# Kernel optimization log

Hardware: AMD Instinct MI355X
Metric: run time of the kernel (lower is better)

Reference implementation:

```python
import jax, jax.numpy as jnp
import numpy as np

D_MODEL = 1024
H = 16
D_K = D_MODEL // H
THETA = 10000.0
MAX_SEQ = 2048
SEQ = 2048
BATCH = 2


def _rope_tables():
    # tri[i, k] angles: i / theta**(2k/d_k)
    pos = jnp.arange(MAX_SEQ, dtype=jnp.float32)[:, None]          # [S, 1]
    inv_freq = THETA ** (-2.0 * jnp.arange(D_K // 2, dtype=jnp.float32) / D_K)  # [dk/2]
    ang = pos * inv_freq                                            # [S, dk/2]
    return jnp.cos(ang), jnp.sin(ang)


def _apply_rope(x, token_positions, cos_t, sin_t):
    # x: [b, h, s, dk]; rotate interleaved pairs
    cos = cos_t[token_positions]  # [s, dk/2]
    sin = sin_t[token_positions]
    x2 = x.reshape(x.shape[:-1] + (D_K // 2, 2))
    x0, x1 = x2[..., 0], x2[..., 1]
    r0 = x0 * cos - x1 * sin
    r1 = x0 * sin + x1 * cos
    return jnp.stack([r0, r1], axis=-1).reshape(x.shape)


def setup_inputs() -> dict:
    key = jax.random.key(0)
    ks = jax.random.split(key, 5)
    sigma = np.sqrt(2.0 / (D_MODEL + D_MODEL))
    return {
        "x": jax.random.normal(ks[0], (BATCH, SEQ, D_MODEL), dtype=jnp.float32),
        "token_positions": jnp.arange(SEQ, dtype=jnp.int64 if jax.config.jax_enable_x64 else jnp.int32),
        "Wq": (jax.random.normal(ks[1], (D_MODEL, D_MODEL), dtype=jnp.float32) * sigma),
        "Wk": (jax.random.normal(ks[2], (D_MODEL, D_MODEL), dtype=jnp.float32) * sigma),
        "Wv": (jax.random.normal(ks[3], (D_MODEL, D_MODEL), dtype=jnp.float32) * sigma),
        "Wo": (jax.random.normal(ks[4], (D_MODEL, D_MODEL), dtype=jnp.float32) * sigma),
    }


def reference(x, token_positions, Wq, Wk, Wv, Wo):
    b, s, _ = x.shape
    cos_t, sin_t = _rope_tables()

    def proj(W):
        y = jnp.einsum('oi,bsi->bso', W, x)                 # [b, s, d_model]
        return y.reshape(b, s, H, D_K).transpose(0, 2, 1, 3)  # [b, h, s, dk]

    Q = _apply_rope(proj(Wq), token_positions, cos_t, sin_t)
    K = _apply_rope(proj(Wk), token_positions, cos_t, sin_t)
    V = proj(Wv)

    scores = jnp.einsum('bhqd,bhkd->bhqk', Q, K) / jnp.sqrt(jnp.float32(D_K))
    causal = jnp.tril(jnp.ones((s, s), dtype=bool))
    scores = jnp.where(causal, scores, -jnp.inf)
    attn = jax.nn.softmax(scores, axis=-1)
    out = jnp.einsum('bhqk,bhkd->bhqd', attn, V)            # [b, h, s, dv]
    out = out.transpose(0, 2, 1, 3).reshape(b, s, D_MODEL)
    return jnp.einsum('oi,bsi->bso', Wo, out)
```

## Files before the change

kernel.cpp:

```cpp
#include <hip/hip_runtime.h>
#include <hip/hip_bf16.h>
#include <math.h>

#define D_MODEL 1024
#define NH      16
#define DK      64
#define SEQ     2048
#define BATCH   2

typedef float  f32x4  __attribute__((ext_vector_type(4)));
typedef __bf16 bf16x8 __attribute__((ext_vector_type(8)));
typedef unsigned short ushx4 __attribute__((ext_vector_type(4)));
typedef unsigned short ushx8 __attribute__((ext_vector_type(8)));
typedef unsigned short u16;

__device__ inline u16 cbf(float f) { __bf16 h = (__bf16)f; return *(u16*)&h; }

__device__ inline void gload16(const u16* g, u16* l) {
    __builtin_amdgcn_global_load_lds(
        (const __attribute__((address_space(1))) unsigned int*)g,
        (__attribute__((address_space(3))) unsigned int*)l,
        16, 0, 0);
}

__global__ void rope_tables_kernel(float* __restrict__ cost, float* __restrict__ sint) {
    int i = blockIdx.x * 256 + threadIdx.x;
    int pos = i >> 5, k = i & 31;
    float inv = powf(10000.0f, -2.0f * (float)k / 64.0f);
    float ang = (float)pos * inv;
    cost[i] = cosf(ang);
    sint[i] = sinf(ang);
}

__global__ void cvt_kernel(const float* __restrict__ in, u16* __restrict__ out) {
    size_t i = ((size_t)blockIdx.x * 256 + threadIdx.x) * 8;
    f32x4 v0 = *(const f32x4*)(in + i);
    f32x4 v1 = *(const f32x4*)(in + i + 4);
    ushx4 o0, o1;
    #pragma unroll
    for (int e = 0; e < 4; e++) { o0[e] = cbf(v0[e]); o1[e] = cbf(v1[e]); }
    *(ushx4*)(out + i) = o0;
    *(ushx4*)(out + i + 4) = o1;
}

__global__ void cvtw_kernel(const float* __restrict__ wq, const float* __restrict__ wk,
                            const float* __restrict__ wv, const float* __restrict__ wo,
                            u16* __restrict__ oq, u16* __restrict__ ok,
                            u16* __restrict__ ov, u16* __restrict__ oo) {
    const float* in; u16* out;
    switch (blockIdx.y) {
        case 0: in = wq; out = oq; break;
        case 1: in = wk; out = ok; break;
        case 2: in = wv; out = ov; break;
        default: in = wo; out = oo; break;
    }
    size_t i = ((size_t)blockIdx.x * 256 + threadIdx.x) * 8;
    f32x4 v0 = *(const f32x4*)(in + i);
    f32x4 v1 = *(const f32x4*)(in + i + 4);
    ushx4 o0, o1;
    #pragma unroll
    for (int e = 0; e < 4; e++) { o0[e] = cbf(v0[e]); o1[e] = cbf(v1[e]); }
    *(ushx4*)(out + i) = o0;
    *(ushx4*)(out + i + 4) = o1;
}

__global__ __launch_bounds__(256) void gemm_qkv(
    const u16* __restrict__ A, const u16* __restrict__ Wqkv,
    u16* __restrict__ Qo, u16* __restrict__ Ko, u16* __restrict__ Vo,
    const int* __restrict__ tpos,
    const float* __restrict__ cost, const float* __restrict__ sint)
{
    constexpr int K = 1024;
    __shared__ u16 As[128 * 64];
    __shared__ u16 Bs[128 * 64];

    const int t  = threadIdx.x;
    const int m0 = blockIdx.x * 128, n0 = blockIdx.y * 128;
    const int lane = t & 63, wid = t >> 6;
    const int wm = wid >> 1, wn = wid & 1;
    const int lr = lane & 15, lg = lane >> 4;
    const int sr = lane >> 3, sc = lane & 7;

    const u16* Asrc[4]; const u16* Bsrc[4];
    #pragma unroll
    for (int i = 0; i < 4; i++) {
        int row = wid * 32 + i * 8 + sr;
        Asrc[i] = A    + (size_t)(m0 + row) * K + ((sc ^ sr) << 3);
        Bsrc[i] = Wqkv + (size_t)(n0 + row) * K + ((sc ^ sr) << 3);
    }

    f32x4 acc[4][4];
    #pragma unroll
    for (int i = 0; i < 4; i++)
        #pragma unroll
        for (int j2 = 0; j2 < 4; j2++) acc[i][j2] = 0.0f;

    for (int k0 = 0; k0 < K; k0 += 64) {
        __syncthreads();
        #pragma unroll
        for (int i = 0; i < 4; i++) gload16(Asrc[i] + k0, &As[(wid * 32 + i * 8) * 64]);
        #pragma unroll
        for (int i = 0; i < 4; i++) gload16(Bsrc[i] + k0, &Bs[(wid * 32 + i * 8) * 64]);
        __syncthreads();

        #pragma unroll
        for (int s = 0; s < 2; s++) {
            bf16x8 af[4], bfr[4];
            #pragma unroll
            for (int mi = 0; mi < 4; mi++) {
                int row = wm * 64 + mi * 16 + lr;
                af[mi] = *(const bf16x8*)&As[row * 64 + (((s * 4 + lg) ^ (lr & 7)) << 3)];
            }
            #pragma unroll
            for (int ni = 0; ni < 4; ni++) {
                int row = wn * 64 + ni * 16 + lr;
                bfr[ni] = *(const bf16x8*)&Bs[row * 64 + (((s * 4 + lg) ^ (lr & 7)) << 3)];
            }
            #pragma unroll
            for (int mi = 0; mi < 4; mi++)
                #pragma unroll
                for (int ni = 0; ni < 4; ni++)
                    acc[mi][ni] = __builtin_amdgcn_mfma_f32_16x16x32_bf16(af[mi], bfr[ni], acc[mi][ni], 0, 0, 0);
        }
    }

    const int sel = n0 >> 10;
    #pragma unroll
    for (int mi = 0; mi < 4; mi++)
        #pragma unroll
        for (int ni = 0; ni < 4; ni++) {
            f32x4 v4 = acc[mi][ni];
            #pragma unroll
            for (int r = 0; r < 4; r++) {
                int m = m0 + wm * 64 + mi * 16 + lg * 4 + r;
                int n = n0 + wn * 64 + ni * 16 + lr;
                float v = v4[r];
                int b = m >> 11, s = m & 2047;
                int h = (n >> 6) & 15, d = n & 63;
                if (sel == 2) {
                    Vo[(((size_t)b * NH + h) * DK + d) * SEQ + s] = cbf(v);
                } else {
                    float vp = __shfl_xor(v, 1);
                    int tp = tpos[s];
                    float c  = cost[tp * 32 + (d >> 1)];
                    float sn = sint[tp * 32 + (d >> 1)];
                    float res = (d & 1) ? (vp * sn + v * c) : (v * c - vp * sn);
                    if (sel == 0) res *= 0.18033688f;
                    u16* outp = sel ? Ko : Qo;
                    outp[(((size_t)b * NH + h) * SEQ + s) * DK + d] = cbf(res);
                }
            }
        }
}

__global__ __launch_bounds__(256) void gemm_out(
    const u16* __restrict__ A, const u16* __restrict__ W, float* __restrict__ outp)
{
    constexpr int K = 1024;
    __shared__ u16 As[128 * 64];
    __shared__ u16 Bs[128 * 64];

    const int t  = threadIdx.x;
    const int m0 = blockIdx.x * 128, n0 = blockIdx.y * 128;
    const int lane = t & 63, wid = t >> 6;
    const int wm = wid >> 1, wn = wid & 1;
    const int lr = lane & 15, lg = lane >> 4;
    const int sr = lane >> 3, sc = lane & 7;

    const u16* Asrc[4]; const u16* Bsrc[4];
    #pragma unroll
    for (int i = 0; i < 4; i++) {
        int row = wid * 32 + i * 8 + sr;
        Asrc[i] = A + (size_t)(m0 + row) * K + ((sc ^ sr) << 3);
        Bsrc[i] = W + (size_t)(n0 + row) * K + ((sc ^ sr) << 3);
    }

    f32x4 acc[4][4];
    #pragma unroll
    for (int i = 0; i < 4; i++)
        #pragma unroll
        for (int j2 = 0; j2 < 4; j2++) acc[i][j2] = 0.0f;

    for (int k0 = 0; k0 < K; k0 += 64) {
        __syncthreads();
        #pragma unroll
        for (int i = 0; i < 4; i++) gload16(Asrc[i] + k0, &As[(wid * 32 + i * 8) * 64]);
        #pragma unroll
        for (int i = 0; i < 4; i++) gload16(Bsrc[i] + k0, &Bs[(wid * 32 + i * 8) * 64]);
        __syncthreads();

        #pragma unroll
        for (int s = 0; s < 2; s++) {
            bf16x8 af[4], bfr[4];
            #pragma unroll
            for (int mi = 0; mi < 4; mi++) {
                int row = wm * 64 + mi * 16 + lr;
                af[mi] = *(const bf16x8*)&As[row * 64 + (((s * 4 + lg) ^ (lr & 7)) << 3)];
            }
            #pragma unroll
            for (int ni = 0; ni < 4; ni++) {
                int row = wn * 64 + ni * 16 + lr;
                bfr[ni] = *(const bf16x8*)&Bs[row * 64 + (((s * 4 + lg) ^ (lr & 7)) << 3)];
            }
            #pragma unroll
            for (int mi = 0; mi < 4; mi++)
                #pragma unroll
                for (int ni = 0; ni < 4; ni++)
                    acc[mi][ni] = __builtin_amdgcn_mfma_f32_16x16x32_bf16(af[mi], bfr[ni], acc[mi][ni], 0, 0, 0);
        }
    }

    #pragma unroll
    for (int mi = 0; mi < 4; mi++)
        #pragma unroll
        for (int ni = 0; ni < 4; ni++) {
            f32x4 v4 = acc[mi][ni];
            #pragma unroll
            for (int r = 0; r < 4; r++) {
                int m = m0 + wm * 64 + mi * 16 + lg * 4 + r;
                int n = n0 + wn * 64 + ni * 16 + lr;
                outp[(size_t)m * D_MODEL + n] = v4[r];
            }
        }
}

__global__ __launch_bounds__(256) void attn_kernel(
    const u16* __restrict__ Q,
    const u16* __restrict__ Km,
    const u16* __restrict__ VT,
    u16* __restrict__ aout)
{
    __shared__ u16 Ks[2][64 * 64];
    __shared__ u16 Vs[64 * 64];
    __shared__ u16 Pl[4][16 * 64];
    const int t = threadIdx.x, wid = t >> 6, lane = t & 63;
    const int lr = lane & 15, lg = lane >> 4;
    const int bx = blockIdx.x;
    const int j = bx & 31;
    const int qb = 31 - (bx >> 5);
    const int bh = (j & 7) * 4 + (j >> 3);
    const int b = bh >> 4, h = bh & 15;
    const int q0 = qb * 64;
    const int qw = q0 + wid * 16;
    const int nkt = qb + 1;
    const int srow = lane >> 3, schunk = lane & 7;

    const u16* Qg = Q  + (size_t)bh * SEQ * DK;
    const u16* Kg = Km + (size_t)bh * SEQ * DK;
    const u16* Vg = VT + (size_t)bh * DK * SEQ;
    u16* Plw = Pl[wid];

    bf16x8 aq[2];
    #pragma unroll
    for (int h2 = 0; h2 < 2; h2++)
        aq[h2] = *(const bf16x8*)&Qg[(qw + lr) * DK + h2 * 32 + lg * 8];

    float m_run = -__builtin_inff(), l_run = 0.0f;
    f32x4 acc[4];
    #pragma unroll
    for (int dg = 0; dg < 4; dg++) acc[dg] = 0.0f;

    auto stageK = [&](int buf, int kb) {
        const int row0 = wid * 16;
        const u16* ks = Kg + (size_t)(kb + row0 + srow) * DK + ((schunk ^ srow) << 3);
        gload16(ks,          &Ks[buf][row0 * 64]);
        gload16(ks + 8 * DK, &Ks[buf][(row0 + 8) * 64]);
    };
    auto stageV = [&](int kb) {
        const int row0 = wid * 16;
        const u16* vs = Vg + (size_t)(row0 + srow) * SEQ + kb + ((schunk ^ srow) << 3);
        gload16(vs,                   &Vs[row0 * 64]);
        gload16(vs + (size_t)8 * SEQ, &Vs[(row0 + 8) * 64]);
    };

    stageK(0, 0);
    for (int kt = 0; kt < nkt; kt++) {
        __builtin_amdgcn_sched_barrier(0);
        __builtin_amdgcn_s_barrier();
        __builtin_amdgcn_sched_barrier(0);
        stageV(kt * 64);
        stageK((kt + 1) & 1, (kt + 1 < nkt) ? (kt + 1) * 64 : 0);
        const int kb = kt * 64;

        asm volatile("s_waitcnt vmcnt(4)" ::: "memory");
        __builtin_amdgcn_sched_barrier(0);
        bf16x8 kf[4][2];
        #pragma unroll
        for (int kg = 0; kg < 4; kg++)
            #pragma unroll
            for (int h2 = 0; h2 < 2; h2++) {
                int row = kg * 16 + lr;
                kf[kg][h2] = *(const bf16x8*)&Ks[kt & 1][row * 64 + (((h2 * 4 + lg) ^ (lr & 7)) << 3)];
            }

        f32x4 sf[4];
        #pragma unroll
        for (int kg = 0; kg < 4; kg++) sf[kg] = 0.0f;
        __builtin_amdgcn_s_setprio(1);
        #pragma unroll
        for (int kg = 0; kg < 4; kg++) {
            sf[kg] = __builtin_amdgcn_mfma_f32_16x16x32_bf16(kf[kg][0], aq[0], sf[kg], 0, 0, 0);
            sf[kg] = __builtin_amdgcn_mfma_f32_16x16x32_bf16(kf[kg][1], aq[1], sf[kg], 0, 0, 0);
        }
        __builtin_amdgcn_s_setprio(0);

        {
            if (kb + 64 > qw) {
                const int qq = qw + lr;
                #pragma unroll
                for (int kg = 0; kg < 4; kg++)
                    #pragma unroll
                    for (int r = 0; r < 4; r++)
                        if (kb + kg * 16 + lg * 4 + r > qq) sf[kg][r] = -__builtin_inff();
            }
            float cmax = sf[0][0];
            #pragma unroll
            for (int kg = 0; kg < 4; kg++)
                #pragma unroll
                for (int r = 0; r < 4; r++) cmax = fmaxf(cmax, sf[kg][r]);
            if (!__all(cmax <= m_run + 8.0f)) {
                float mt = fmaxf(cmax, __shfl_xor(cmax, 16));
                mt = fmaxf(mt, __shfl_xor(mt, 32));
                float mn = fmaxf(m_run, mt);
                float scr = exp2f(m_run - mn);
                m_run = mn;
                l_run *= scr;
                #pragma unroll
                for (int dg = 0; dg < 4; dg++) acc[dg] *= scr;
            }
            float l = 0.0f;
            const int prow = lr * 64;
            #pragma unroll
            for (int kg = 0; kg < 4; kg++) {
                ushx4 pk;
                #pragma unroll
                for (int r = 0; r < 4; r++) {
                    float p = exp2f(sf[kg][r] - m_run);
                    l += p;
                    pk[r] = cbf(p);
                }
                *(ushx4*)&Plw[prow + (((kg * 4 + lg) ^ ((lr & 7) << 1)) << 2)] = pk;
            }
            l_run += l;
        }

        asm volatile("s_waitcnt vmcnt(2)" ::: "memory");
        __builtin_amdgcn_sched_barrier(0);
        bf16x8 vf[2][4];
        #pragma unroll
        for (int ck = 0; ck < 2; ck++)
            #pragma unroll
            for (int dg = 0; dg < 4; dg++) {
                int row = dg * 16 + lr;
                vf[ck][dg] = *(const bf16x8*)&Vs[row * 64 + (((ck * 4 + lg) ^ (lr & 7)) << 3)];
            }

        asm volatile("s_waitcnt lgkmcnt(0)" ::: "memory");
        __builtin_amdgcn_sched_barrier(0);
        bf16x8 pa[2];
        #pragma unroll
        for (int ck = 0; ck < 2; ck++)
            pa[ck] = *(const bf16x8*)&Plw[lr * 64 + (((ck * 8 + lg * 2) ^ ((lr & 7) << 1)) << 2)];
        __builtin_amdgcn_s_setprio(1);
        #pragma unroll
        for (int ck = 0; ck < 2; ck++)
            #pragma unroll
            for (int dg = 0; dg < 4; dg++)
                acc[dg] = __builtin_amdgcn_mfma_f32_16x16x32_bf16(vf[ck][dg], pa[ck], acc[dg], 0, 0, 0);
        __builtin_amdgcn_s_setprio(0);
    }

    l_run += __shfl_xor(l_run, 16);
    l_run += __shfl_xor(l_run, 32);

    {
        float inv = 1.0f / l_run;
        int q = qw + lr;
        #pragma unroll
        for (int dg = 0; dg < 4; dg++) {
            ushx4 ow;
            #pragma unroll
            for (int r = 0; r < 4; r++) ow[r] = cbf(acc[dg][r] * inv);
            *(ushx4*)&aout[((size_t)b * SEQ + q) * D_MODEL + h * DK + dg * 16 + lg * 4] = ow;
        }
    }
}

extern "C" void kernel_launch(void* const* d_in, const int* in_sizes, int n_in,
                              void* d_out, int out_size, void* d_ws, size_t ws_size,
                              hipStream_t stream) {
    const float* x    = (const float*)d_in[0];
    const int*   tpos = (const int*)d_in[1];
    const float* Wq   = (const float*)d_in[2];
    const float* Wk   = (const float*)d_in[3];
    const float* Wv   = (const float*)d_in[4];
    const float* Wo   = (const float*)d_in[5];
    float* out = (float*)d_out;

    char* ws = (char*)d_ws;
    float* cost = (float*)ws;
    float* sint = (float*)(ws + (256 << 10));
    u16* Qb   = (u16*)(ws + (512 << 10));
    u16* Kb   = (u16*)(ws + (512 << 10) + ((size_t)8  << 20));
    u16* VT   = (u16*)(ws + (512 << 10) + ((size_t)16 << 20));
    u16* xb   = (u16*)(ws + (512 << 10) + ((size_t)24 << 20));
    u16* Wqb  = (u16*)(ws + (512 << 10) + ((size_t)32 << 20));
    u16* Wkb  = (u16*)(ws + (512 << 10) + ((size_t)34 << 20));
    u16* Wvb  = (u16*)(ws + (512 << 10) + ((size_t)36 << 20));
    u16* Wob  = (u16*)(ws + (512 << 10) + ((size_t)38 << 20));
    u16* attnb = xb;

    rope_tables_kernel<<<256, 256, 0, stream>>>(cost, sint);
    cvt_kernel<<<2048, 256, 0, stream>>>(x, xb);
    cvtw_kernel<<<dim3(512, 4), 256, 0, stream>>>(Wq, Wk, Wv, Wo, Wqb, Wkb, Wvb, Wob);

    gemm_qkv<<<dim3(32, 24), 256, 0, stream>>>(xb, Wqb, Qb, Kb, VT, tpos, cost, sint);

    attn_kernel<<<1024, 256, 0, stream>>>(Qb, Kb, VT, attnb);

    gemm_out<<<dim3(32, 8), 256, 0, stream>>>(attnb, Wob, out);
}
```

Before: 148.7 us.

## Double-buffer GEMM K-loop and transpose V-projection via swapped MFMA operands

Unifies the QKV and output GEMMs into one templated kernel. The K-loop now uses a 32-wide double-buffered LDS stage, prefetching the next tile while computing the current one, with a single barrier per iteration. The V projection is split into its own launch that swaps the MFMA operands, so each lane holds consecutive sequence positions and the transposed V store is less scattered. The cos and sin RoPE tables are interleaved into a float2 table so one load fetches both. The cost is twice as many loop iterations with smaller tiles, and one extra kernel launch.

```diff
diff --git a/kernel.cpp b/kernel.cpp
--- a/kernel.cpp
+++ b/kernel.cpp
@@ -23,13 +23,12 @@
         16, 0, 0);
 }
 
-__global__ void rope_tables_kernel(float* __restrict__ cost, float* __restrict__ sint) {
+__global__ void rope_tables_kernel(float2* __restrict__ cs) {
     int i = blockIdx.x * 256 + threadIdx.x;
     int pos = i >> 5, k = i & 31;
     float inv = powf(10000.0f, -2.0f * (float)k / 64.0f);
     float ang = (float)pos * inv;
-    cost[i] = cosf(ang);
-    sint[i] = sinf(ang);
+    cs[i] = make_float2(cosf(ang), sinf(ang));
 }
 
 __global__ void cvt_kernel(const float* __restrict__ in, u16* __restrict__ out) {
@@ -64,67 +63,73 @@
     *(ushx4*)(out + i + 4) = o1;
 }
 
-__global__ __launch_bounds__(256) void gemm_qkv(
-    const u16* __restrict__ A, const u16* __restrict__ Wqkv,
-    u16* __restrict__ Qo, u16* __restrict__ Ko, u16* __restrict__ Vo,
-    const int* __restrict__ tpos,
-    const float* __restrict__ cost, const float* __restrict__ sint)
+template<int MODE>
+__global__ __launch_bounds__(256) void gemm_bt(
+    const u16* __restrict__ A, const u16* __restrict__ W,
+    u16* __restrict__ Qo, u16* __restrict__ Ko, void* __restrict__ Oo,
+    const int* __restrict__ tpos, const float2* __restrict__ cs)
 {
     constexpr int K = 1024;
-    __shared__ u16 As[128 * 64];
-    __shared__ u16 Bs[128 * 64];
+    __shared__ u16 As[2][128 * 32];
+    __shared__ u16 Bs[2][128 * 32];
 
     const int t  = threadIdx.x;
     const int m0 = blockIdx.x * 128, n0 = blockIdx.y * 128;
     const int lane = t & 63, wid = t >> 6;
     const int wm = wid >> 1, wn = wid & 1;
     const int lr = lane & 15, lg = lane >> 4;
-    const int sr = lane >> 3, sc = lane & 7;
-
-    const u16* Asrc[4]; const u16* Bsrc[4];
-    #pragma unroll
-    for (int i = 0; i < 4; i++) {
-        int row = wid * 32 + i * 8 + sr;
-        Asrc[i] = A    + (size_t)(m0 + row) * K + ((sc ^ sr) << 3);
-        Bsrc[i] = Wqkv + (size_t)(n0 + row) * K + ((sc ^ sr) << 3);
+
+    const int ldrow0 = wid * 32 + (lane >> 2);
+    const int ldrow1 = ldrow0 + 16;
+    const int lc = lane & 3;
+    const u16* Asrc0 = A + (size_t)(m0 + ldrow0) * K + ((lc ^ ((ldrow0 >> 1) & 3)) << 3);
+    const u16* Asrc1 = A + (size_t)(m0 + ldrow1) * K + ((lc ^ ((ldrow1 >> 1) & 3)) << 3);
+    const u16* Bsrc0 = W + (size_t)(n0 + ldrow0) * K + ((lc ^ ((ldrow0 >> 1) & 3)) << 3);
+    const u16* Bsrc1 = W + (size_t)(n0 + ldrow1) * K + ((lc ^ ((ldrow1 >> 1) & 3)) << 3);
+    const int d0 = (wid * 32) * 32, d1 = (wid * 32 + 16) * 32;
+
+    f32x4 acc[4][4];
+    #pragma unroll
+    for (int i = 0; i < 4; i++)
+        #pragma unroll
+        for (int j2 = 0; j2 < 4; j2++) acc[i][j2] = 0.0f;
+
+    auto stage = [&](int buf, int k0) {
+        gload16(Asrc0 + k0, &As[buf][d0]);
+        gload16(Asrc1 + k0, &As[buf][d1]);
+        gload16(Bsrc0 + k0, &Bs[buf][d0]);
+        gload16(Bsrc1 + k0, &Bs[buf][d1]);
+    };
+
+    stage(0, 0);
+    int buf = 0;
+    for (int k0 = 0; k0 < K; k0 += 32) {
+        __syncthreads();
+        if (k0 + 32 < K) stage(buf ^ 1, k0 + 32);
+
+        bf16x8 af[4], bfr[4];
+        #pragma unroll
+        for (int mi = 0; mi < 4; mi++) {
+            int row = wm * 64 + mi * 16 + lr;
+            af[mi] = *(const bf16x8*)&As[buf][row * 32 + ((lg ^ ((row >> 1) & 3)) << 3)];
+        }
+        #pragma unroll
+        for (int ni = 0; ni < 4; ni++) {
+            int row = wn * 64 + ni * 16 + lr;
+            bfr[ni] = *(const bf16x8*)&Bs[buf][row * 32 + ((lg ^ ((row >> 1) & 3)) << 3)];
+        }
+        #pragma unroll
+        for (int mi = 0; mi < 4; mi++)
+            #pragma unroll
+            for (int ni = 0; ni < 4; ni++) {
+                if constexpr (MODE == 3)
+                    acc[mi][ni] = __builtin_amdgcn_mfma_f32_16x16x32_bf16(bfr[ni], af[mi], acc[mi][ni], 0, 0, 0);
+                else
+                    acc[mi][ni] = __builtin_amdgcn_mfma_f32_16x16x32_bf16(af[mi], bfr[ni], acc[mi][ni], 0, 0, 0);
+            }
+        buf ^= 1;
     }
 
-    f32x4 acc[4][4];
-    #pragma unroll
-    for (int i = 0; i < 4; i++)
-        #pragma unroll
-        for (int j2 = 0; j2 < 4; j2++) acc[i][j2] = 0.0f;
-
-    for (int k0 = 0; k0 < K; k0 += 64) {
-        __syncthreads();
-        #pragma unroll
-        for (int i = 0; i < 4; i++) gload16(Asrc[i] + k0, &As[(wid * 32 + i * 8) * 64]);
-        #pragma unroll
-        for (int i = 0; i < 4; i++) gload16(Bsrc[i] + k0, &Bs[(wid * 32 + i * 8) * 64]);
-        __syncthreads();
-
-        #pragma unroll
-        for (int s = 0; s < 2; s++) {
-            bf16x8 af[4], bfr[4];
-            #pragma unroll
-            for (int mi = 0; mi < 4; mi++) {
-                int row = wm * 64 + mi * 16 + lr;
-                af[mi] = *(const bf16x8*)&As[row * 64 + (((s * 4 + lg) ^ (lr & 7)) << 3)];
-            }
-            #pragma unroll
-            for (int ni = 0; ni < 4; ni++) {
-                int row = wn * 64 + ni * 16 + lr;
-                bfr[ni] = *(const bf16x8*)&Bs[row * 64 + (((s * 4 + lg) ^ (lr & 7)) << 3)];
-            }
-            #pragma unroll
-            for (int mi = 0; mi < 4; mi++)
-                #pragma unroll
-                for (int ni = 0; ni < 4; ni++)
-                    acc[mi][ni] = __builtin_amdgcn_mfma_f32_16x16x32_bf16(af[mi], bfr[ni], acc[mi][ni], 0, 0, 0);
-        }
-    }
-
-    const int sel = n0 >> 10;
     #pragma unroll
     for (int mi = 0; mi < 4; mi++)
         #pragma unroll
@@ -132,94 +137,31 @@
             f32x4 v4 = acc[mi][ni];
             #pragma unroll
             for (int r = 0; r < 4; r++) {
-                int m = m0 + wm * 64 + mi * 16 + lg * 4 + r;
-                int n = n0 + wn * 64 + ni * 16 + lr;
                 float v = v4[r];
-                int b = m >> 11, s = m & 2047;
-                int h = (n >> 6) & 15, d = n & 63;
-                if (sel == 2) {
-                    Vo[(((size_t)b * NH + h) * DK + d) * SEQ + s] = cbf(v);
+                if constexpr (MODE == 3) {
+                    int n = n0 + wn * 64 + ni * 16 + lg * 4 + r;
+                    int m = m0 + wm * 64 + mi * 16 + lr;
+                    int h = n >> 6, d = n & 63;
+                    int b = m >> 11, s = m & 2047;
+                    ((u16*)Oo)[(((size_t)b * NH + h) * DK + d) * SEQ + s] = cbf(v);
                 } else {
-                    float vp = __shfl_xor(v, 1);
-                    int tp = tpos[s];
-                    float c  = cost[tp * 32 + (d >> 1)];
-                    float sn = sint[tp * 32 + (d >> 1)];
-                    float res = (d & 1) ? (vp * sn + v * c) : (v * c - vp * sn);
-                    if (sel == 0) res *= 0.18033688f;
-                    u16* outp = sel ? Ko : Qo;
-                    outp[(((size_t)b * NH + h) * SEQ + s) * DK + d] = cbf(res);
+                    int m = m0 + wm * 64 + mi * 16 + lg * 4 + r;
+                    int n = n0 + wn * 64 + ni * 16 + lr;
+                    if constexpr (MODE == 2) {
+                        ((float*)Oo)[(size_t)m * D_MODEL + n] = v;
+                    } else {
+                        int b = m >> 11, s = m & 2047;
+                        int h = (n >> 6) & 15, d = n & 63;
+                        float vp = __shfl_xor(v, 1);
+                        int tp = tpos[s];
+                        float2 c2 = cs[tp * 32 + (d >> 1)];
+                        float res = (d & 1) ? (vp * c2.y + v * c2.x) : (v * c2.x - vp * c2.y);
+                        const int sel = n0 >> 10;
+                        if (sel == 0) res *= 0.18033688f;
+                        u16* outp = sel ? Ko : Qo;
+                        outp[(((size_t)b * NH + h) * SEQ + s) * DK + d] = cbf(res);
+                    }
                 }
-            }
-        }
-}
-
-__global__ __launch_bounds__(256) void gemm_out(
-    const u16* __restrict__ A, const u16* __restrict__ W, float* __restrict__ outp)
-{
-    constexpr int K = 1024;
-    __shared__ u16 As[128 * 64];
-    __shared__ u16 Bs[128 * 64];
-
-    const int t  = threadIdx.x;
-    const int m0 = blockIdx.x * 128, n0 = blockIdx.y * 128;
-    const int lane = t & 63, wid = t >> 6;
-    const int wm = wid >> 1, wn = wid & 1;
-    const int lr = lane & 15, lg = lane >> 4;
-    const int sr = lane >> 3, sc = lane & 7;
-
-    const u16* Asrc[4]; const u16* Bsrc[4];
-    #pragma unroll
-    for (int i = 0; i < 4; i++) {
-        int row = wid * 32 + i * 8 + sr;
-        Asrc[i] = A + (size_t)(m0 + row) * K + ((sc ^ sr) << 3);
-        Bsrc[i] = W + (size_t)(n0 + row) * K + ((sc ^ sr) << 3);
-    }
-
-    f32x4 acc[4][4];
-    #pragma unroll
-    for (int i = 0; i < 4; i++)
-        #pragma unroll
-        for (int j2 = 0; j2 < 4; j2++) acc[i][j2] = 0.0f;
-
-    for (int k0 = 0; k0 < K; k0 += 64) {
-        __syncthreads();
-        #pragma unroll
-        for (int i = 0; i < 4; i++) gload16(Asrc[i] + k0, &As[(wid * 32 + i * 8) * 64]);
-        #pragma unroll
-        for (int i = 0; i < 4; i++) gload16(Bsrc[i] + k0, &Bs[(wid * 32 + i * 8) * 64]);
-        __syncthreads();
-
-        #pragma unroll
-        for (int s = 0; s < 2; s++) {
-            bf16x8 af[4], bfr[4];
-            #pragma unroll
-            for (int mi = 0; mi < 4; mi++) {
-                int row = wm * 64 + mi * 16 + lr;
-                af[mi] = *(const bf16x8*)&As[row * 64 + (((s * 4 + lg) ^ (lr & 7)) << 3)];
-            }
-            #pragma unroll
-            for (int ni = 0; ni < 4; ni++) {
-                int row = wn * 64 + ni * 16 + lr;
-                bfr[ni] = *(const bf16x8*)&Bs[row * 64 + (((s * 4 + lg) ^ (lr & 7)) << 3)];
-            }
-            #pragma unroll
-            for (int mi = 0; mi < 4; mi++)
-                #pragma unroll
-                for (int ni = 0; ni < 4; ni++)
-                    acc[mi][ni] = __builtin_amdgcn_mfma_f32_16x16x32_bf16(af[mi], bfr[ni], acc[mi][ni], 0, 0, 0);
-        }
-    }
-
-    #pragma unroll
-    for (int mi = 0; mi < 4; mi++)
-        #pragma unroll
-        for (int ni = 0; ni < 4; ni++) {
-            f32x4 v4 = acc[mi][ni];
-            #pragma unroll
-            for (int r = 0; r < 4; r++) {
-                int m = m0 + wm * 64 + mi * 16 + lg * 4 + r;
-                int n = n0 + wn * 64 + ni * 16 + lr;
-                outp[(size_t)m * D_MODEL + n] = v4[r];
             }
         }
 }
@@ -398,8 +340,7 @@
     float* out = (float*)d_out;
 
     char* ws = (char*)d_ws;
-    float* cost = (float*)ws;
-    float* sint = (float*)(ws + (256 << 10));
+    float2* cs = (float2*)ws;
     u16* Qb   = (u16*)(ws + (512 << 10));
     u16* Kb   = (u16*)(ws + (512 << 10) + ((size_t)8  << 20));
     u16* VT   = (u16*)(ws + (512 << 10) + ((size_t)16 << 20));
@@ -410,13 +351,14 @@
     u16* Wob  = (u16*)(ws + (512 << 10) + ((size_t)38 << 20));
     u16* attnb = xb;
 
-    rope_tables_kernel<<<256, 256, 0, stream>>>(cost, sint);
+    rope_tables_kernel<<<256, 256, 0, stream>>>(cs);
     cvt_kernel<<<2048, 256, 0, stream>>>(x, xb);
     cvtw_kernel<<<dim3(512, 4), 256, 0, stream>>>(Wq, Wk, Wv, Wo, Wqb, Wkb, Wvb, Wob);
 
-    gemm_qkv<<<dim3(32, 24), 256, 0, stream>>>(xb, Wqb, Qb, Kb, VT, tpos, cost, sint);
+    gemm_bt<0><<<dim3(32, 16), 256, 0, stream>>>(xb, Wqb, Qb, Kb, nullptr, tpos, cs);
+    gemm_bt<3><<<dim3(32, 8),  256, 0, stream>>>(xb, Wvb, nullptr, nullptr, VT, tpos, cs);
 
     attn_kernel<<<1024, 256, 0, stream>>>(Qb, Kb, VT, attnb);
 
-    gemm_out<<<dim3(32, 8), 256, 0, stream>>>(attnb, Wob, out);
-}
+    gemm_bt<2><<<dim3(32, 8),  256, 0, stream>>>(attnb, Wob, nullptr, nullptr, out, tpos, cs);
+}
```

Result: faster. 131.1 us (-11.8%).
